# Optimization experiments

Measured on AMD Instinct MI355X. Metric: run time of the kernel, lower is better.

Reference implementation:

```python
import jax, jax.numpy as jnp
import numpy as np


def setup_inputs() -> dict:
    key = jax.random.key(0)
    k1, k2, k3 = jax.random.split(key, 3)
    inp = jax.random.normal(k1, (32, 128, 56, 56), dtype=jnp.float32)
    # kaiming-style scale for a 3x3 conv kernel
    fan_in = 128 * 3 * 3
    kernel = jax.random.normal(k2, (256, 128, 3, 3), dtype=jnp.float32) * np.float32(np.sqrt(2.0 / fan_in))
    bias = jax.random.normal(k3, (256,), dtype=jnp.float32)
    return {"inp": inp, "kernel": kernel, "bias": bias}


def reference(inp, kernel, bias):
    # 3x3 conv, stride 1, padding 1 (SAME), NCHW / OIHW layout, plus bias.
    out = jax.lax.conv_general_dilated(
        inp, kernel,
        window_strides=(1, 1),
        padding=((1, 1), (1, 1)),
        dimension_numbers=("NCHW", "OIHW", "NCHW"),
    )
    return out + bias[None, :, None, None]
```

## Files before the change

### kernel.cpp

```cpp
#include <hip/hip_runtime.h>
#include <hip/hip_bf16.h>
#include <stdint.h>


#define C_IN   128
#define K_OUT  256
#define HW     56
#define IMG    3136
#define NBATCH 32
#define SPATIAL 100352
#define PW     58
#define PADTOT (NBATCH*PW*PW*C_IN)
#define KTOT   1152

typedef __bf16 bf16x8 __attribute__((ext_vector_type(8)));
typedef float  f32x4  __attribute__((ext_vector_type(4)));

__device__ inline unsigned short f2bf(float f) {
    unsigned int u = __builtin_bit_cast(unsigned int, f);
    u += ((u >> 16) & 1u) + 0x7FFFu;
    return (unsigned short)(u >> 16);
}

__device__ __forceinline__ void gl2lds16(const unsigned short* g, unsigned short* l) {
    __builtin_amdgcn_global_load_lds(
        (const __attribute__((address_space(1))) unsigned int*)g,
        (__attribute__((address_space(3))) unsigned int*)l, 16, 0, 0);
}

__global__ void prep_input(const float* __restrict__ inp,
                           unsigned short* __restrict__ dst) {
    __shared__ unsigned short tile[C_IN * 57];
    int n = blockIdx.x / PW, py = blockIdx.x % PW;
    unsigned short* d = dst + (size_t)blockIdx.x * (PW * C_IN);
    if (py == 0 || py == PW - 1) {
        for (int i = threadIdx.x; i < PW * C_IN; i += 256) d[i] = 0;
        return;
    }
    const float* src = inp + (size_t)n * C_IN * IMG + (py - 1) * HW;
    for (int i = threadIdx.x; i < C_IN * HW; i += 256) {
        int c = i / HW, x = i - c * HW;
        tile[c * 57 + x] = f2bf(src[c * IMG + x]);
    }
    __syncthreads();
    for (int i = threadIdx.x; i < PW * C_IN; i += 256) {
        int px = i >> 7, c = i & 127;
        unsigned short v = 0;
        if (px >= 1 && px <= HW) v = tile[c * 57 + (px - 1)];
        d[i] = v;
    }
}

__global__ void prep_weights(const float* __restrict__ w,
                             unsigned short* __restrict__ dst) {
    int idx = blockIdx.x * 256 + threadIdx.x;
    int ko = idx / KTOT, rem = idx - ko * KTOT;
    int rs = rem >> 7, c = rem & 127;
    dst[idx] = f2bf(w[(ko * C_IN + c) * 9 + rs]);
}

__global__ __launch_bounds__(256) void conv_mfma(
        const unsigned short* __restrict__ In,
        const unsigned short* __restrict__ Wt,
        const float* __restrict__ bias,
        float* __restrict__ out) {
    __shared__ unsigned short smem[16384];

    const int tid = threadIdx.x;
    const int lane = tid & 63, w = tid >> 6;
    const int wr = w >> 1, wc = w & 1;
    const int l15 = lane & 15, lk = lane >> 4;
    const int lr = lane >> 3, lj = lane & 7;
    const int jd = lj ^ lr;

    const int pblk0 = blockIdx.x * 128;
    const int ko0   = blockIdx.y * 128;

    int eA[4]; int pbq[4];
#pragma unroll
    for (int qi = 0; qi < 4; ++qi) {
        int row = 32 * w + 8 * qi + lr;
        eA[qi] = (ko0 + row) * KTOT + jd * 8;
        int p = pblk0 + row;
        int n = p / IMG; int rem = p - n * IMG;
        int y = rem / HW; int x = rem - y * HW;
        pbq[qi] = ((n * PW + y) * PW + x) * C_IN + jd * 8;
    }

    f32x4 acc[4][4];
#pragma unroll
    for (int m = 0; m < 4; ++m)
#pragma unroll
        for (int n = 0; n < 4; ++n) acc[m][n] = (f32x4)0.0f;

    const int jx0   = lk ^ (l15 & 7);
    const int aBase = (wr * 64 + l15) * 128;
    const int bBase = 16384 + (wc * 64 + l15) * 128;
    const char* sm = (const char*)smem;

#pragma unroll
    for (int kt = 0; kt < 18; ++kt) {
        const int rs = kt >> 1;
        const int r = rs / 3, s = rs - 3 * (rs / 3);
        const int goff = (r * PW + s) * C_IN + (kt & 1) * 64;
#pragma unroll
        for (int qi = 0; qi < 4; ++qi)
            gl2lds16(Wt + eA[qi] + kt * 64, &smem[(4 * w + qi) * 512]);
#pragma unroll
        for (int qi = 0; qi < 4; ++qi)
            gl2lds16(In + pbq[qi] + goff, &smem[8192 + (4 * w + qi) * 512]);
        __syncthreads();
#pragma unroll
        for (int ks = 0; ks < 2; ++ks) {
            const int jo = (jx0 ^ (ks ? 4 : 0)) * 16;
            bf16x8 a[4], b[4];
#pragma unroll
            for (int m = 0; m < 4; ++m)
                a[m] = *(const bf16x8*)(sm + aBase + m * 2048 + jo);
#pragma unroll
            for (int n = 0; n < 4; ++n)
                b[n] = *(const bf16x8*)(sm + bBase + n * 2048 + jo);
#pragma unroll
            for (int m = 0; m < 4; ++m)
#pragma unroll
                for (int n = 0; n < 4; ++n)
                    acc[m][n] = __builtin_amdgcn_mfma_f32_16x16x32_bf16(
                        a[m], b[n], acc[m][n], 0, 0, 0);
        }
        __syncthreads();
    }

    const int jrow = lk * 4;
#pragma unroll
    for (int m = 0; m < 4; ++m) {
        int kb = ko0 + wr * 64 + m * 16 + jrow;
        f32x4 bs = *(const f32x4*)(bias + kb);
#pragma unroll
        for (int nf = 0; nf < 4; ++nf) {
            int p = pblk0 + wc * 64 + nf * 16 + l15;
            int ni = p / IMG; int spi = p - ni * IMG;
            float* ob = out + (size_t)(ni * K_OUT + kb) * IMG + spi;
#pragma unroll
            for (int j = 0; j < 4; ++j)
                ob[j * IMG] = acc[m][nf][j] + bs[j];
        }
    }
}

__global__ void conv_naive(const float* __restrict__ inp,
                           const float* __restrict__ ker,
                           const float* __restrict__ bias,
                           float* __restrict__ out, int total) {
    int o = blockIdx.x * blockDim.x + threadIdx.x;
    if (o >= total) return;
    int x = o % HW, y = (o / HW) % HW, ko = (o / IMG) % K_OUT, n = o / (IMG * K_OUT);
    float acc = bias[ko];
    for (int c = 0; c < C_IN; ++c)
        for (int r = 0; r < 3; ++r) {
            int iy = y + r - 1; if ((unsigned)iy >= HW) continue;
            for (int s = 0; s < 3; ++s) {
                int ix = x + s - 1; if ((unsigned)ix >= HW) continue;
                acc += inp[((n * C_IN + c) * HW + iy) * HW + ix]
                     * ker[((ko * C_IN + c) * 3 + r) * 3 + s];
            }
        }
    out[o] = acc;
}

extern "C" void kernel_launch(void* const* d_in, const int* in_sizes, int n_in,
                              void* d_out, int out_size, void* d_ws, size_t ws_size,
                              hipStream_t stream) {
    const float* inp  = (const float*)d_in[0];
    const float* ker  = (const float*)d_in[1];
    const float* bias = (const float*)d_in[2];
    float* out = (float*)d_out;

    const size_t need = (size_t)PADTOT * 2 + (size_t)K_OUT * KTOT * 2;
    if (ws_size < need) {
        int total = NBATCH * K_OUT * IMG;
        conv_naive<<<(total + 255) / 256, 256, 0, stream>>>(inp, ker, bias, out, total);
        return;
    }

    unsigned short* inb = (unsigned short*)d_ws;
    unsigned short* wtb = inb + (size_t)PADTOT;

    prep_input<<<NBATCH * PW, 256, 0, stream>>>(inp, inb);
    prep_weights<<<(K_OUT * KTOT) / 256, 256, 0, stream>>>(ker, wtb);

    dim3 grid(SPATIAL / 128, K_OUT / 128);
    conv_mfma<<<grid, 256, 0, stream>>>(inb, wtb, bias, out);
}
```

Measured before the change: 96.56 us.

## Restructure conv as row-tile implicit GEMM with halo reuse and double-buffered staging

The main conv kernel now runs 512 threads per block. Each block covers all 256 output channels for four image rows, loading the padded input rows once into LDS and reusing them across the 3x3 taps instead of re-gathering im2col tiles for every tap. Weight and input slices are double-buffered in about 144KB of LDS, with explicit vmcnt waits and s_setprio so the next loads overlap the MFMAs. The input prep also writes 8-wide vectors. The large LDS footprint and heavy accumulator use limit occupancy, and the 448-block grid may not fill the device evenly.

```diff
diff --git a/kernel.cpp b/kernel.cpp
--- a/kernel.cpp
+++ b/kernel.cpp
@@ -1,6 +1,5 @@
 #include <hip/hip_runtime.h>
 #include <hip/hip_bf16.h>
-#include <stdint.h>
 
 
 #define C_IN   128
@@ -15,6 +14,7 @@
 
 typedef __bf16 bf16x8 __attribute__((ext_vector_type(8)));
 typedef float  f32x4  __attribute__((ext_vector_type(4)));
+typedef unsigned short ushort8 __attribute__((ext_vector_type(8)));
 
 __device__ inline unsigned short f2bf(float f) {
     unsigned int u = __builtin_bit_cast(unsigned int, f);
@@ -32,9 +32,9 @@
                            unsigned short* __restrict__ dst) {
     __shared__ unsigned short tile[C_IN * 57];
     int n = blockIdx.x / PW, py = blockIdx.x % PW;
-    unsigned short* d = dst + (size_t)blockIdx.x * (PW * C_IN);
+    ushort8* d8 = (ushort8*)(dst + (size_t)blockIdx.x * (PW * C_IN));
     if (py == 0 || py == PW - 1) {
-        for (int i = threadIdx.x; i < PW * C_IN; i += 256) d[i] = 0;
+        for (int i = threadIdx.x; i < PW * C_IN / 8; i += 256) d8[i] = (ushort8)0;
         return;
     }
     const float* src = inp + (size_t)n * C_IN * IMG + (py - 1) * HW;
@@ -43,11 +43,14 @@
         tile[c * 57 + x] = f2bf(src[c * IMG + x]);
     }
     __syncthreads();
-    for (int i = threadIdx.x; i < PW * C_IN; i += 256) {
-        int px = i >> 7, c = i & 127;
-        unsigned short v = 0;
-        if (px >= 1 && px <= HW) v = tile[c * 57 + (px - 1)];
-        d[i] = v;
+    for (int i = threadIdx.x; i < PW * C_IN / 8; i += 256) {
+        int px = i >> 4, c0 = (i & 15) * 8;
+        ushort8 v = (ushort8)0;
+        if (px >= 1 && px <= HW) {
+#pragma unroll
+            for (int e = 0; e < 8; ++e) v[e] = tile[(c0 + e) * 57 + (px - 1)];
+        }
+        d8[i] = v;
     }
 }
 
@@ -59,90 +62,109 @@
     dst[idx] = f2bf(w[(ko * C_IN + c) * 9 + rs]);
 }
 
-__global__ __launch_bounds__(256) void conv_mfma(
+__global__ __launch_bounds__(512, 2) void conv_mfma(
         const unsigned short* __restrict__ In,
         const unsigned short* __restrict__ Wt,
         const float* __restrict__ bias,
         float* __restrict__ out) {
-    __shared__ unsigned short smem[16384];
+    __shared__ unsigned short smem[73728];
 
     const int tid = threadIdx.x;
-    const int lane = tid & 63, w = tid >> 6;
-    const int wr = w >> 1, wc = w & 1;
+    const int lane = tid & 63, wv = tid >> 6;
     const int l15 = lane & 15, lk = lane >> 4;
-    const int lr = lane >> 3, lj = lane & 7;
-    const int jd = lj ^ lr;
-
-    const int pblk0 = blockIdx.x * 128;
-    const int ko0   = blockIdx.y * 128;
-
-    int eA[4]; int pbq[4];
-#pragma unroll
-    for (int qi = 0; qi < 4; ++qi) {
-        int row = 32 * w + 8 * qi + lr;
-        eA[qi] = (ko0 + row) * KTOT + jd * 8;
-        int p = pblk0 + row;
-        int n = p / IMG; int rem = p - n * IMG;
-        int y = rem / HW; int x = rem - y * HW;
-        pbq[qi] = ((n * PW + y) * PW + x) * C_IN + jd * 8;
-    }
-
-    f32x4 acc[4][4];
+    const int blk = blockIdx.x;
+    const int n = blk / 14, rb = (blk % 14) * 4;
+
+    const int wko = (wv & 3) * 64;
+    const int wpx = (wv >> 2) * 112;
+    const int albase = l15 * 64 + lk * 16;
+
+    int rowoff[7];
+#pragma unroll
+    for (int nf = 0; nf < 7; ++nf) {
+        int p = wpx + nf * 16 + l15;
+        int yl = p / 56, x = p - yl * 56;
+        rowoff[nf] = (yl * 58 + x) * 64 + lk * 16;
+    }
+
+    f32x4 acc[4][7];
 #pragma unroll
     for (int m = 0; m < 4; ++m)
 #pragma unroll
-        for (int n = 0; n < 4; ++n) acc[m][n] = (f32x4)0.0f;
-
-    const int jx0   = lk ^ (l15 & 7);
-    const int aBase = (wr * 64 + l15) * 128;
-    const int bBase = 16384 + (wc * 64 + l15) * 128;
-    const char* sm = (const char*)smem;
-
-#pragma unroll
-    for (int kt = 0; kt < 18; ++kt) {
-        const int rs = kt >> 1;
-        const int r = rs / 3, s = rs - 3 * (rs / 3);
-        const int goff = (r * PW + s) * C_IN + (kt & 1) * 64;
-#pragma unroll
-        for (int qi = 0; qi < 4; ++qi)
-            gl2lds16(Wt + eA[qi] + kt * 64, &smem[(4 * w + qi) * 512]);
-#pragma unroll
-        for (int qi = 0; qi < 4; ++qi)
-            gl2lds16(In + pbq[qi] + goff, &smem[8192 + (4 * w + qi) * 512]);
-        __syncthreads();
-#pragma unroll
-        for (int ks = 0; ks < 2; ++ks) {
-            const int jo = (jx0 ^ (ks ? 4 : 0)) * 16;
-            bf16x8 a[4], b[4];
-#pragma unroll
-            for (int m = 0; m < 4; ++m)
-                a[m] = *(const bf16x8*)(sm + aBase + m * 2048 + jo);
-#pragma unroll
-            for (int n = 0; n < 4; ++n)
-                b[n] = *(const bf16x8*)(sm + bBase + n * 2048 + jo);
-#pragma unroll
-            for (int m = 0; m < 4; ++m)
-#pragma unroll
-                for (int n = 0; n < 4; ++n)
-                    acc[m][n] = __builtin_amdgcn_mfma_f32_16x16x32_bf16(
-                        a[m], b[n], acc[m][n], 0, 0, 0);
-        }
-        __syncthreads();
-    }
-
-    const int jrow = lk * 4;
+        for (int nf = 0; nf < 7; ++nf) acc[m][nf] = (f32x4)0.0f;
+
+#define STAGE_W(PHN, RN, CQN) do {                                          \
+    _Pragma("unroll")                                                       \
+    for (int li = 0; li < 6; ++li) {                                        \
+        int chunk = li * 512 + tid;                                         \
+        int s_ = chunk >> 10, rem_ = chunk & 1023;                          \
+        int ko_ = rem_ >> 2, cc_ = rem_ & 3;                                \
+        gl2lds16(Wt + ko_ * KTOT + ((RN) * 3 + s_) * 128 + (CQN) * 32 + cc_ * 8, \
+                 &smem[((PHN) & 1) * 24576 + chunk * 8]);                   \
+    } } while (0)
+
+#define STAGE_I(CQN, R_) do {                                               \
+    int chunk = (R_) * 512 + tid;                                           \
+    int ch2 = chunk < 1392 ? chunk : 0;                                     \
+    int t_ = ch2 / 232, rem_ = ch2 - t_ * 232;                              \
+    int X_ = rem_ >> 2, cc_ = rem_ & 3;                                     \
+    gl2lds16(In + (((n * 58 + rb + t_) * 58 + X_) * 128) + (CQN) * 32 + cc_ * 8, \
+             &smem[49152 + ((CQN) & 1) * 12288 + chunk * 8]);               \
+} while (0)
+
+    STAGE_W(0, 0, 0);
+    STAGE_I(0, 0); STAGE_I(0, 1); STAGE_I(0, 2);
+
+#define PHASE(PH) do {                                                      \
+    constexpr int cq_ = (PH) / 3, r_ = (PH) % 3;                            \
+    if ((PH) < 11) { STAGE_W((PH) + 1, ((PH) + 1) % 3, ((PH) + 1) / 3); }   \
+    if (cq_ < 3)   { STAGE_I(cq_ + 1, r_); }                                \
+    asm volatile("s_waitcnt vmcnt(%0)"                                      \
+                 :: "i"((PH) < 9 ? 7 : ((PH) < 11 ? 6 : 0)) : "memory");    \
+    __builtin_amdgcn_s_barrier();                                           \
+    { const char* wb = (const char*)smem + ((PH) & 1) * 49152;              \
+      const char* ib = (const char*)smem + 98304 + (cq_ & 1) * 24576;       \
+      __builtin_amdgcn_s_setprio(1);                                        \
+      _Pragma("unroll")                                                     \
+      for (int s = 0; s < 3; ++s) {                                         \
+          bf16x8 a[4], b[7];                                                \
+          _Pragma("unroll")                                                 \
+          for (int m = 0; m < 4; ++m)                                       \
+              a[m] = *(const bf16x8*)(wb + s * 16384 + (wko + m * 16) * 64 + albase); \
+          _Pragma("unroll")                                                 \
+          for (int nf = 0; nf < 7; ++nf)                                    \
+              b[nf] = *(const bf16x8*)(ib + rowoff[nf] + (r_ * 58 + s) * 64); \
+          _Pragma("unroll")                                                 \
+          for (int m = 0; m < 4; ++m)                                       \
+              _Pragma("unroll")                                             \
+              for (int nf = 0; nf < 7; ++nf)                                \
+                  acc[m][nf] = __builtin_amdgcn_mfma_f32_16x16x32_bf16(     \
+                      a[m], b[nf], acc[m][nf], 0, 0, 0);                    \
+      }                                                                     \
+      __builtin_amdgcn_s_setprio(0);                                        \
+    }                                                                       \
+    __builtin_amdgcn_s_barrier();                                           \
+} while (0)
+
+    PHASE(0);  PHASE(1);  PHASE(2);  PHASE(3);
+    PHASE(4);  PHASE(5);  PHASE(6);  PHASE(7);
+    PHASE(8);  PHASE(9);  PHASE(10); PHASE(11);
+
+#undef PHASE
+#undef STAGE_I
+#undef STAGE_W
+
+    const int sp0 = rb * 56 + wpx;
 #pragma unroll
     for (int m = 0; m < 4; ++m) {
-        int kb = ko0 + wr * 64 + m * 16 + jrow;
+        int kb = wko + m * 16 + lk * 4;
         f32x4 bs = *(const f32x4*)(bias + kb);
 #pragma unroll
-        for (int nf = 0; nf < 4; ++nf) {
-            int p = pblk0 + wc * 64 + nf * 16 + l15;
-            int ni = p / IMG; int spi = p - ni * IMG;
-            float* ob = out + (size_t)(ni * K_OUT + kb) * IMG + spi;
+        for (int nf = 0; nf < 7; ++nf) {
+            float* ob = out + ((size_t)(n * K_OUT + kb) * IMG) + sp0 + nf * 16 + l15;
 #pragma unroll
             for (int j = 0; j < 4; ++j)
-                ob[j * IMG] = acc[m][nf][j] + bs[j];
+                ob[(size_t)j * IMG] = acc[m][nf][j] + bs[j];
         }
     }
 }
@@ -188,6 +210,5 @@
     prep_input<<<NBATCH * PW, 256, 0, stream>>>(inp, inb);
     prep_weights<<<(K_OUT * KTOT) / 256, 256, 0, stream>>>(ker, wtb);
 
-    dim3 grid(SPATIAL / 128, K_OUT / 128);
-    conv_mfma<<<grid, 256, 0, stream>>>(inb, wtb, bias, out);
-}
+    conv_mfma<<<448, 512, 0, stream>>>(inb, wtb, bias, out);
+}
```

Result: faster. 91.07 us (-5.7%).
